# Optimization experiments

Hardware: AMD Instinct MI355X
Metric: run time of the kernel (lower is better)

Reference implementation:

```python
import jax, jax.numpy as jnp
import numpy as np

U = 128  # linear_units

def setup_inputs() -> dict:
    key = jax.random.key(0)
    k1, k2, k3, k4, k5, k6 = jax.random.split(key, 6)
    B, S, D = 16, 2048, 128
    x = jax.random.normal(k1, (B, S, D), dtype=jnp.float32)
    t = jax.random.uniform(k2, (B, S), dtype=jnp.float32)
    # glorot_uniform inits
    lim_qk = np.sqrt(6.0 / (D + U)).astype(np.float32)
    Wq = jax.random.uniform(k3, (D, U), minval=-lim_qk, maxval=lim_qk, dtype=jnp.float32)
    Wk = jax.random.uniform(k4, (D, U), minval=-lim_qk, maxval=lim_qk, dtype=jnp.float32)
    lim_s = np.sqrt(6.0 / (1 + S)).astype(np.float32)
    theta = jax.random.uniform(k5, (1, S), minval=-lim_s, maxval=lim_s, dtype=jnp.float32)
    mu = jax.random.uniform(k6, (1, S), minval=-lim_s, maxval=lim_s, dtype=jnp.float32)
    return {"x": x, "t": t, "Wq": Wq, "Wk": Wk, "theta": theta, "mu": mu}

def reference(x, t, Wq, Wk, theta, mu):
    # x: (B,S,D), t: (B,S), theta/mu: (1,S)
    scale = jnp.sqrt(jnp.asarray(U, dtype=x.dtype))
    q = x @ Wq                                   # (B,S,U)
    k = x @ Wk                                   # (B,S,U)
    scores = jnp.einsum('biu,bju->bij', q, k) / scale  # (B,S,S)
    alphas = jax.nn.softmax(scores, axis=-1)
    gn = jnp.einsum('bij,bjd->bid', alphas, x)   # weighted sum == alphas @ x, (B,S,D)
    time_fact = jax.nn.sigmoid(theta - mu * t)   # (B,S)
    v = jnp.sum(gn * time_fact[:, :, None], axis=1)  # (B,D)
    return v
```

## Files before the change

kernel.cpp:

```cpp
#include <hip/hip_runtime.h>
#include <hip/hip_bf16.h>

#define SS 2048
#define DD 128
#define BB 16
#define LDST 136
#define SCT 268

typedef short bf16x8 __attribute__((ext_vector_type(8)));
typedef float f32x4 __attribute__((ext_vector_type(4)));
typedef unsigned short ushort_t;

#define SB0() __builtin_amdgcn_sched_barrier(0)
#define WAITV(n) asm volatile("s_waitcnt vmcnt(" #n ")" ::: "memory")

__device__ __forceinline__ unsigned short f2bf(float f) {
  union { float f; unsigned u; } v; v.f = f;
  unsigned r = v.u + 0x7fffu + ((v.u >> 16) & 1u);
  return (unsigned short)(r >> 16);
}
__device__ __forceinline__ float fexp2(float x) { return __builtin_amdgcn_exp2f(x); }


__global__ __launch_bounds__(256) void wprep(
    const float* __restrict__ Wq, const float* __restrict__ Wk,
    ushort_t* __restrict__ wt_g) {
  int idx = blockIdx.x * 256 + threadIdx.x;
  int r = idx & 16383, uu = r >> 7, d = r & 127;
  if (idx < 16384)
    wt_g[uu * 128 + d] = f2bf(Wq[d * 128 + uu] * 0.1275174346f);
  else
    wt_g[(uu + 128) * 128 + d] = f2bf(Wk[d * 128 + uu]);
}

__global__ __launch_bounds__(256, 2) void qk_gemm(
    const float* __restrict__ x, const ushort_t* __restrict__ wt_g,
    uint4* __restrict__ qF, uint4* __restrict__ kF) {
  __shared__ ushort_t xs[64 * LDST];
  __shared__ ushort_t sc[64 * SCT];
  const int tid = threadIdx.x, wave = tid >> 6, lane = tid & 63;
  const int lq = lane & 15, quad = lane >> 4;
  const int m0 = blockIdx.x * 64;

#pragma unroll
  for (int i = 0; i < 8; ++i) {
    int idx = i * 256 + tid;
    int row = idx >> 5, c4 = (idx & 31) * 4;
    const float4 v = *(const float4*)(x + (size_t)(m0 + row) * DD + c4);
    ushort4 h;
    h.x = f2bf(v.x); h.y = f2bf(v.y); h.z = f2bf(v.z); h.w = f2bf(v.w);
    *(ushort4*)(&xs[row * LDST + c4]) = h;
  }
  bf16x8 wf[4][4];
#pragma unroll
  for (int nt = 0; nt < 4; ++nt)
#pragma unroll
    for (int ks = 0; ks < 4; ++ks)
      wf[nt][ks] = *(const bf16x8*)(wt_g + (wave * 64 + nt * 16 + lq) * 128 + ks * 32 + quad * 8);
  __syncthreads();

  f32x4 acc[4][4];
#pragma unroll
  for (int mt = 0; mt < 4; ++mt)
#pragma unroll
    for (int nt = 0; nt < 4; ++nt) acc[mt][nt] = (f32x4){0.f, 0.f, 0.f, 0.f};
#pragma unroll
  for (int mt = 0; mt < 4; ++mt) {
    bf16x8 af[4];
#pragma unroll
    for (int ks = 0; ks < 4; ++ks)
      af[ks] = *(const bf16x8*)(&xs[(mt * 16 + lq) * LDST + ks * 32 + quad * 8]);
#pragma unroll
    for (int nt = 0; nt < 4; ++nt)
#pragma unroll
      for (int ks = 0; ks < 4; ++ks)
        acc[mt][nt] = __builtin_amdgcn_mfma_f32_16x16x32_bf16(af[ks], wf[nt][ks], acc[mt][nt], 0, 0, 0);
  }
#pragma unroll
  for (int mt = 0; mt < 4; ++mt)
#pragma unroll
    for (int nt = 0; nt < 4; ++nt)
#pragma unroll
      for (int r = 0; r < 4; ++r)
        sc[(mt * 16 + quad * 4 + r) * SCT + wave * 64 + nt * 16 + lq] = f2bf(acc[mt][nt][r]);
  __syncthreads();
#pragma unroll
  for (int i = 0; i < 8; ++i) {
    int c = i * 256 + tid;
    int lane_c = c & 63, ks_c = (c >> 6) & 3, g_c = (c >> 8) & 3, isk = c >> 10;
    int li = lane_c & 15, qd = lane_c >> 4;
    int col = isk * 128 + ks_c * 32 + qd * 8;
    uint4 v = *(const uint4*)(&sc[(g_c * 16 + li) * SCT + col]);
    size_t G = (size_t)blockIdx.x * 4 + g_c;
    uint4* dst = isk ? kF : qF;
    dst[(G * 4 + ks_c) * 64 + lane_c] = v;
  }
}

__global__ __launch_bounds__(256, 2) void attn_fused(
    const uint4* __restrict__ qF, const uint4* __restrict__ kF,
    const float* __restrict__ t, const float* __restrict__ theta,
    const float* __restrict__ mu, float* __restrict__ w) {
  const int xcd = blockIdx.x & 7, s = blockIdx.x >> 3;
  const int b = xcd + ((s >> 5) << 3);
  const int ib = s & 31;
  const int i0 = ib * 64;
  const int tid = threadIdx.x, wave = tid >> 6, lane = tid & 63;
  const int lq = lane & 15, quad = lane >> 4;

  __shared__ float rs_lds[4][64];
  __shared__ float c_lds[64];

  const bf16x8* qc = (const bf16x8*)qF;

  bf16x8 af[4][4];
#pragma unroll
  for (int mt = 0; mt < 4; ++mt)
#pragma unroll
    for (int ks = 0; ks < 4; ++ks)
      af[mt][ks] = qc[((size_t)(b * 128 + ib * 4 + mt) * 4 + ks) * 64 + lane];

  const bf16x8* kb = (const bf16x8*)kF + (size_t)b * 128 * 4 * 64 + lane;
  auto loadg = [&](bf16x8 (&f)[4], int g) {
#pragma unroll
    for (int ks = 0; ks < 4; ++ks)
      f[ks] = kb[((size_t)g * 4 + ks) * 64];
  };
  auto G = [&](int m) { return (m >> 1) * 8 + wave * 2 + (m & 1); };

  const f32x4 z4 = {0.f, 0.f, 0.f, 0.f};
  auto mfma16 = [&](f32x4 (&a)[4], bf16x8 (&f)[4]) {
    __builtin_amdgcn_s_setprio(1);
#pragma unroll
    for (int mt = 0; mt < 4; ++mt)
      a[mt] = __builtin_amdgcn_mfma_f32_16x16x32_bf16(af[mt][0], f[0], z4, 0, 0, 0);
#pragma unroll
    for (int ks = 1; ks < 4; ++ks)
#pragma unroll
      for (int mt = 0; mt < 4; ++mt)
        a[mt] = __builtin_amdgcn_mfma_f32_16x16x32_bf16(af[mt][ks], f[ks], a[mt], 0, 0, 0);
    __builtin_amdgcn_s_setprio(0);
  };

  float rowsum[4][4];
#pragma unroll
  for (int mt = 0; mt < 4; ++mt)
#pragma unroll
    for (int r = 0; r < 4; ++r) rowsum[mt][r] = 0.f;
  auto proc1 = [&](f32x4 (&a)[4]) {
#pragma unroll
    for (int mt = 0; mt < 4; ++mt)
#pragma unroll
      for (int r = 0; r < 4; ++r) rowsum[mt][r] += fexp2(a[mt][r]);
  };

  bf16x8 fA[4], fB[4];
  f32x4 a[4];

  loadg(fA, G(0));
  loadg(fB, G(1));
  for (int m = 0; m < 30; m += 2) {
    WAITV(4); SB0();
    mfma16(a, fA);
    loadg(fA, G(m + 2)); SB0();
    proc1(a);
    WAITV(4); SB0();
    mfma16(a, fB);
    loadg(fB, G(m + 3)); SB0();
    proc1(a);
  }
  WAITV(4); SB0(); mfma16(a, fA); SB0(); proc1(a);
  WAITV(0); SB0(); mfma16(a, fB); SB0(); proc1(a);

#pragma unroll
  for (int d2 = 1; d2 <= 8; d2 <<= 1)
#pragma unroll
    for (int mt = 0; mt < 4; ++mt)
#pragma unroll
      for (int r = 0; r < 4; ++r)
        rowsum[mt][r] += __shfl_xor(rowsum[mt][r], d2, 64);
  if (lq == 0) {
#pragma unroll
    for (int mt = 0; mt < 4; ++mt)
#pragma unroll
      for (int r = 0; r < 4; ++r)
        rs_lds[wave][mt * 16 + quad * 4 + r] = rowsum[mt][r];
  }
  __syncthreads();
  if (tid < 64) {
    float l = rs_lds[0][tid] + rs_lds[1][tid] + rs_lds[2][tid] + rs_lds[3][tid];
    int gi = i0 + tid;
    float z = theta[gi] - mu[gi] * t[b * SS + gi];
    float tf = 1.f / (1.f + fexp2(-z * 1.44269504f));
    c_lds[tid] = tf / l;
  }
  __syncthreads();
  float creg[4][4];
#pragma unroll
  for (int mt = 0; mt < 4; ++mt)
#pragma unroll
    for (int r = 0; r < 4; ++r) creg[mt][r] = c_lds[mt * 16 + quad * 4 + r];

  auto proc2 = [&](f32x4 (&aa)[4], int g) {
    float cs = 0.f;
#pragma unroll
    for (int mt = 0; mt < 4; ++mt)
#pragma unroll
      for (int r = 0; r < 4; ++r) cs = fmaf(creg[mt][r], fexp2(aa[mt][r]), cs);
    cs += __shfl_xor(cs, 16, 64);
    cs += __shfl_xor(cs, 32, 64);
    if (lane < 16) atomicAdd(&w[b * SS + g * 16 + lane], cs);
  };

  loadg(fA, G(0));
  loadg(fB, G(1));
  for (int m = 0; m < 30; m += 2) {
    WAITV(4); SB0();
    mfma16(a, fA);
    loadg(fA, G(m + 2)); SB0();
    proc2(a, G(m));
    WAITV(4); SB0();
    mfma16(a, fB);
    loadg(fB, G(m + 3)); SB0();
    proc2(a, G(m + 1));
  }
  WAITV(4); SB0(); mfma16(a, fA); SB0(); proc2(a, G(30));
  WAITV(0); SB0(); mfma16(a, fB); SB0(); proc2(a, G(31));
}

__global__ __launch_bounds__(256) void finalize(
    const float* __restrict__ x, const float* __restrict__ w,
    float* __restrict__ out) {
  const int b = blockIdx.x >> 5;
  const int j0 = (blockIdx.x & 31) * 64;
  const int tid = threadIdx.x;
  const int d4 = (tid & 31) * 4, jo = tid >> 5;
  float4 a0 = {0.f, 0.f, 0.f, 0.f}, a1 = {0.f, 0.f, 0.f, 0.f};
#pragma unroll
  for (int jj = 0; jj < 4; ++jj) {
    int ja = j0 + jj * 16 + jo, jb = ja + 8;
    float wa = w[b * SS + ja], wb = w[b * SS + jb];
    const float4 xa = *(const float4*)(x + ((size_t)b * SS + ja) * DD + d4);
    const float4 xb = *(const float4*)(x + ((size_t)b * SS + jb) * DD + d4);
    a0.x = fmaf(wa, xa.x, a0.x); a0.y = fmaf(wa, xa.y, a0.y);
    a0.z = fmaf(wa, xa.z, a0.z); a0.w = fmaf(wa, xa.w, a0.w);
    a1.x = fmaf(wb, xb.x, a1.x); a1.y = fmaf(wb, xb.y, a1.y);
    a1.z = fmaf(wb, xb.z, a1.z); a1.w = fmaf(wb, xb.w, a1.w);
  }
  __shared__ float4 red[256];
  float4 acc = {a0.x + a1.x, a0.y + a1.y, a0.z + a1.z, a0.w + a1.w};
  red[tid] = acc;
  __syncthreads();
  if (tid < 128) {
    float4 o = red[tid + 128];
    red[tid].x += o.x; red[tid].y += o.y; red[tid].z += o.z; red[tid].w += o.w;
  }
  __syncthreads();
  if (tid < 64) {
    float4 o = red[tid + 64];
    red[tid].x += o.x; red[tid].y += o.y; red[tid].z += o.z; red[tid].w += o.w;
  }
  __syncthreads();
  if (tid < 32) {
    float4 v = red[tid], o = red[tid + 32];
    v.x += o.x; v.y += o.y; v.z += o.z; v.w += o.w;
    atomicAdd(&out[b * DD + d4 + 0], v.x);
    atomicAdd(&out[b * DD + d4 + 1], v.y);
    atomicAdd(&out[b * DD + d4 + 2], v.z);
    atomicAdd(&out[b * DD + d4 + 3], v.w);
  }
}

extern "C" void kernel_launch(void* const* d_in, const int* in_sizes, int n_in,
                              void* d_out, int out_size, void* d_ws, size_t ws_size,
                              hipStream_t stream) {
  const float* x = (const float*)d_in[0];
  const float* t = (const float*)d_in[1];
  const float* Wq = (const float*)d_in[2];
  const float* Wk = (const float*)d_in[3];
  const float* theta = (const float*)d_in[4];
  const float* mu = (const float*)d_in[5];
  float* out = (float*)d_out;

  uint4* qF = (uint4*)d_ws;
  uint4* kF = qF + (size_t)2048 * 4 * 64;
  ushort_t* wt_g = (ushort_t*)(kF + (size_t)2048 * 4 * 64);
  float* w = (float*)(wt_g + 256 * 128);

  hipMemsetAsync(w, 0, (size_t)BB * SS * sizeof(float), stream);
  hipMemsetAsync(d_out, 0, (size_t)BB * DD * sizeof(float), stream);

  wprep<<<dim3(128), dim3(256), 0, stream>>>(Wq, Wk, wt_g);
  qk_gemm<<<dim3(512), dim3(256), 0, stream>>>(x, wt_g, qF, kF);
  attn_fused<<<dim3(512), dim3(256), 0, stream>>>(qF, kF, t, theta, mu, w);
  finalize<<<dim3(512), dim3(256), 0, stream>>>(x, w, out);
}
```

Measured before the change: 127.2 us.

## Switch attention score MFMAs to 32x32x16 tiles with matching fragment layout

The attention kernel now uses 32x32x16 bf16 MFMA instructions instead of 16x16x32. The q/k fragment layout written by qk_gemm changes to match, and the row-sum and weight reductions are remapped to the 32-lane layout. Larger tiles reduce the instruction count and give more reuse per operand load, while the column atomics now cover 32 entries per wave step. Separately, wprep is rewritten as an LDS-tiled transpose over 8 blocks to coalesce weight reads. The costs are higher register pressure (8 K fragments per buffer, 16-float accumulators) and more complex index mapping.

```diff
diff --git a/kernel.cpp b/kernel.cpp
--- a/kernel.cpp
+++ b/kernel.cpp
@@ -9,6 +9,7 @@
 
 typedef short bf16x8 __attribute__((ext_vector_type(8)));
 typedef float f32x4 __attribute__((ext_vector_type(4)));
+typedef float f32x16 __attribute__((ext_vector_type(16)));
 typedef unsigned short ushort_t;
 
 #define SB0() __builtin_amdgcn_sched_barrier(0)
@@ -25,12 +26,29 @@
 __global__ __launch_bounds__(256) void wprep(
     const float* __restrict__ Wq, const float* __restrict__ Wk,
     ushort_t* __restrict__ wt_g) {
-  int idx = blockIdx.x * 256 + threadIdx.x;
-  int r = idx & 16383, uu = r >> 7, d = r & 127;
-  if (idx < 16384)
-    wt_g[uu * 128 + d] = f2bf(Wq[d * 128 + uu] * 0.1275174346f);
-  else
-    wt_g[(uu + 128) * 128 + d] = f2bf(Wk[d * 128 + uu]);
+  const int isK = blockIdx.x >> 2, ut = (blockIdx.x >> 1) & 1, dt = blockIdx.x & 1;
+  const int tid = threadIdx.x;
+  const float* W = isK ? Wk : Wq;
+  const float scale = isK ? 1.0f : 0.1275174346f;
+  __shared__ float tile[64][65];
+  {
+    int uu = tid & 63, dr = tid >> 6;
+#pragma unroll
+    for (int p = 0; p < 16; ++p) {
+      int d = p * 4 + dr;
+      tile[uu][d] = W[(size_t)(dt * 64 + d) * 128 + ut * 64 + uu];
+    }
+  }
+  __syncthreads();
+  {
+    int d = tid & 63, ur = tid >> 6;
+#pragma unroll
+    for (int p = 0; p < 16; ++p) {
+      int uu = p * 4 + ur;
+      wt_g[(size_t)(isK * 128 + ut * 64 + uu) * 128 + dt * 64 + d] =
+          f2bf(tile[uu][d] * scale);
+    }
+  }
 }
 
 __global__ __launch_bounds__(256, 2) void qk_gemm(
@@ -87,13 +105,13 @@
 #pragma unroll
   for (int i = 0; i < 8; ++i) {
     int c = i * 256 + tid;
-    int lane_c = c & 63, ks_c = (c >> 6) & 3, g_c = (c >> 8) & 3, isk = c >> 10;
-    int li = lane_c & 15, qd = lane_c >> 4;
-    int col = isk * 128 + ks_c * 32 + qd * 8;
-    uint4 v = *(const uint4*)(&sc[(g_c * 16 + li) * SCT + col]);
-    size_t G = (size_t)blockIdx.x * 4 + g_c;
+    int lane_c = c & 63, ci = c >> 6;
+    int wv = ci & 7, Hloc = (ci >> 3) & 1, isk = ci >> 4;
+    int row = Hloc * 32 + (lane_c & 31);
+    int col = isk * 128 + wv * 16 + (lane_c >> 5) * 8;
+    uint4 v = *(const uint4*)(&sc[row * SCT + col]);
     uint4* dst = isk ? kF : qF;
-    dst[(G * 4 + ks_c) * 64 + lane_c] = v;
+    dst[((size_t)(blockIdx.x * 2 + Hloc) * 8 + wv) * 64 + lane_c] = v;
   }
 }
 
@@ -106,85 +124,85 @@
   const int ib = s & 31;
   const int i0 = ib * 64;
   const int tid = threadIdx.x, wave = tid >> 6, lane = tid & 63;
-  const int lq = lane & 15, quad = lane >> 4;
+  const int l31 = lane & 31, lh = lane >> 5;
 
   __shared__ float rs_lds[4][64];
   __shared__ float c_lds[64];
 
   const bf16x8* qc = (const bf16x8*)qF;
-
-  bf16x8 af[4][4];
-#pragma unroll
-  for (int mt = 0; mt < 4; ++mt)
-#pragma unroll
-    for (int ks = 0; ks < 4; ++ks)
-      af[mt][ks] = qc[((size_t)(b * 128 + ib * 4 + mt) * 4 + ks) * 64 + lane];
-
-  const bf16x8* kb = (const bf16x8*)kF + (size_t)b * 128 * 4 * 64 + lane;
-  auto loadg = [&](bf16x8 (&f)[4], int g) {
-#pragma unroll
-    for (int ks = 0; ks < 4; ++ks)
-      f[ks] = kb[((size_t)g * 4 + ks) * 64];
+  bf16x8 af[2][8];
+#pragma unroll
+  for (int ht = 0; ht < 2; ++ht)
+#pragma unroll
+    for (int wv = 0; wv < 8; ++wv)
+      af[ht][wv] = qc[((size_t)(b * 64 + ib * 2 + ht) * 8 + wv) * 64 + lane];
+
+  const bf16x8* kb = (const bf16x8*)kF + (size_t)b * 64 * 8 * 64 + lane;
+  auto loadg = [&](bf16x8 (&f)[8], int hj) {
+#pragma unroll
+    for (int wv = 0; wv < 8; ++wv)
+      f[wv] = kb[((size_t)hj * 8 + wv) * 64];
   };
-  auto G = [&](int m) { return (m >> 1) * 8 + wave * 2 + (m & 1); };
-
-  const f32x4 z4 = {0.f, 0.f, 0.f, 0.f};
-  auto mfma16 = [&](f32x4 (&a)[4], bf16x8 (&f)[4]) {
+  auto HJ = [&](int m) { return m * 4 + wave; };
+
+  const f32x16 z16 = {0.f, 0.f, 0.f, 0.f, 0.f, 0.f, 0.f, 0.f,
+                      0.f, 0.f, 0.f, 0.f, 0.f, 0.f, 0.f, 0.f};
+  auto mfma32 = [&](f32x16 (&a)[2], bf16x8 (&f)[8]) {
     __builtin_amdgcn_s_setprio(1);
 #pragma unroll
-    for (int mt = 0; mt < 4; ++mt)
-      a[mt] = __builtin_amdgcn_mfma_f32_16x16x32_bf16(af[mt][0], f[0], z4, 0, 0, 0);
-#pragma unroll
-    for (int ks = 1; ks < 4; ++ks)
-#pragma unroll
-      for (int mt = 0; mt < 4; ++mt)
-        a[mt] = __builtin_amdgcn_mfma_f32_16x16x32_bf16(af[mt][ks], f[ks], a[mt], 0, 0, 0);
+    for (int ht = 0; ht < 2; ++ht)
+      a[ht] = __builtin_amdgcn_mfma_f32_32x32x16_bf16(af[ht][0], f[0], z16, 0, 0, 0);
+#pragma unroll
+    for (int wv = 1; wv < 8; ++wv)
+#pragma unroll
+      for (int ht = 0; ht < 2; ++ht)
+        a[ht] = __builtin_amdgcn_mfma_f32_32x32x16_bf16(af[ht][wv], f[wv], a[ht], 0, 0, 0);
     __builtin_amdgcn_s_setprio(0);
   };
 
-  float rowsum[4][4];
-#pragma unroll
-  for (int mt = 0; mt < 4; ++mt)
-#pragma unroll
-    for (int r = 0; r < 4; ++r) rowsum[mt][r] = 0.f;
-  auto proc1 = [&](f32x4 (&a)[4]) {
-#pragma unroll
-    for (int mt = 0; mt < 4; ++mt)
-#pragma unroll
-      for (int r = 0; r < 4; ++r) rowsum[mt][r] += fexp2(a[mt][r]);
+  float rowsum[2][16];
+#pragma unroll
+  for (int ht = 0; ht < 2; ++ht)
+#pragma unroll
+    for (int r = 0; r < 16; ++r) rowsum[ht][r] = 0.f;
+  auto proc1 = [&](f32x16 (&a)[2]) {
+#pragma unroll
+    for (int ht = 0; ht < 2; ++ht)
+#pragma unroll
+      for (int r = 0; r < 16; ++r) rowsum[ht][r] += fexp2(a[ht][r]);
   };
 
-  bf16x8 fA[4], fB[4];
-  f32x4 a[4];
-
-  loadg(fA, G(0));
-  loadg(fB, G(1));
-  for (int m = 0; m < 30; m += 2) {
-    WAITV(4); SB0();
-    mfma16(a, fA);
-    loadg(fA, G(m + 2)); SB0();
+  bf16x8 fA[8], fB[8];
+  f32x16 a[2];
+
+  loadg(fA, HJ(0));
+  loadg(fB, HJ(1));
+  for (int m = 0; m < 14; m += 2) {
+    WAITV(8); SB0();
+    mfma32(a, fA);
+    loadg(fA, HJ(m + 2)); SB0();
     proc1(a);
-    WAITV(4); SB0();
-    mfma16(a, fB);
-    loadg(fB, G(m + 3)); SB0();
+    WAITV(8); SB0();
+    mfma32(a, fB);
+    loadg(fB, HJ(m + 3)); SB0();
     proc1(a);
   }
-  WAITV(4); SB0(); mfma16(a, fA); SB0(); proc1(a);
-  WAITV(0); SB0(); mfma16(a, fB); SB0(); proc1(a);
-
-#pragma unroll
-  for (int d2 = 1; d2 <= 8; d2 <<= 1)
-#pragma unroll
-    for (int mt = 0; mt < 4; ++mt)
-#pragma unroll
-      for (int r = 0; r < 4; ++r)
-        rowsum[mt][r] += __shfl_xor(rowsum[mt][r], d2, 64);
-  if (lq == 0) {
-#pragma unroll
-    for (int mt = 0; mt < 4; ++mt)
-#pragma unroll
-      for (int r = 0; r < 4; ++r)
-        rs_lds[wave][mt * 16 + quad * 4 + r] = rowsum[mt][r];
+  WAITV(8); SB0(); mfma32(a, fA); SB0(); proc1(a);
+  WAITV(0); SB0(); mfma32(a, fB); SB0(); proc1(a);
+
+#pragma unroll
+  for (int d2 = 1; d2 <= 16; d2 <<= 1)
+#pragma unroll
+    for (int ht = 0; ht < 2; ++ht)
+#pragma unroll
+      for (int r = 0; r < 16; ++r)
+        rowsum[ht][r] += __shfl_xor(rowsum[ht][r], d2, 64);
+  if (l31 == 0) {
+#pragma unroll
+    for (int ht = 0; ht < 2; ++ht)
+#pragma unroll
+      for (int r = 0; r < 16; ++r)
+        rs_lds[wave][ht * 32 + (r & 3) + 8 * (r >> 2) + 4 * lh] = rowsum[ht][r];
   }
   __syncthreads();
   if (tid < 64) {
@@ -195,37 +213,39 @@
     c_lds[tid] = tf / l;
   }
   __syncthreads();
-  float creg[4][4];
-#pragma unroll
-  for (int mt = 0; mt < 4; ++mt)
-#pragma unroll
-    for (int r = 0; r < 4; ++r) creg[mt][r] = c_lds[mt * 16 + quad * 4 + r];
-
-  auto proc2 = [&](f32x4 (&aa)[4], int g) {
-    float cs = 0.f;
-#pragma unroll
-    for (int mt = 0; mt < 4; ++mt)
-#pragma unroll
-      for (int r = 0; r < 4; ++r) cs = fmaf(creg[mt][r], fexp2(aa[mt][r]), cs);
-    cs += __shfl_xor(cs, 16, 64);
+  float creg[2][16];
+#pragma unroll
+  for (int ht = 0; ht < 2; ++ht)
+#pragma unroll
+    for (int r = 0; r < 16; ++r)
+      creg[ht][r] = c_lds[ht * 32 + (r & 3) + 8 * (r >> 2) + 4 * lh];
+
+  auto proc2 = [&](f32x16 (&aa)[2], int hj) {
+    float c0 = 0.f, c1 = 0.f;
+#pragma unroll
+    for (int r = 0; r < 16; ++r) {
+      c0 = fmaf(creg[0][r], fexp2(aa[0][r]), c0);
+      c1 = fmaf(creg[1][r], fexp2(aa[1][r]), c1);
+    }
+    float cs = c0 + c1;
     cs += __shfl_xor(cs, 32, 64);
-    if (lane < 16) atomicAdd(&w[b * SS + g * 16 + lane], cs);
+    if (lane < 32) atomicAdd(&w[b * SS + hj * 32 + l31], cs);
   };
 
-  loadg(fA, G(0));
-  loadg(fB, G(1));
-  for (int m = 0; m < 30; m += 2) {
-    WAITV(4); SB0();
-    mfma16(a, fA);
-    loadg(fA, G(m + 2)); SB0();
-    proc2(a, G(m));
-    WAITV(4); SB0();
-    mfma16(a, fB);
-    loadg(fB, G(m + 3)); SB0();
-    proc2(a, G(m + 1));
-  }
-  WAITV(4); SB0(); mfma16(a, fA); SB0(); proc2(a, G(30));
-  WAITV(0); SB0(); mfma16(a, fB); SB0(); proc2(a, G(31));
+  loadg(fA, HJ(0));
+  loadg(fB, HJ(1));
+  for (int m = 0; m < 14; m += 2) {
+    WAITV(8); SB0();
+    mfma32(a, fA);
+    loadg(fA, HJ(m + 2)); SB0();
+    proc2(a, HJ(m));
+    WAITV(8); SB0();
+    mfma32(a, fB);
+    loadg(fB, HJ(m + 3)); SB0();
+    proc2(a, HJ(m + 1));
+  }
+  WAITV(8); SB0(); mfma32(a, fA); SB0(); proc2(a, HJ(14));
+  WAITV(0); SB0(); mfma32(a, fB); SB0(); proc2(a, HJ(15));
 }
 
 __global__ __launch_bounds__(256) void finalize(
@@ -283,14 +303,14 @@
   float* out = (float*)d_out;
 
   uint4* qF = (uint4*)d_ws;
-  uint4* kF = qF + (size_t)2048 * 4 * 64;
-  ushort_t* wt_g = (ushort_t*)(kF + (size_t)2048 * 4 * 64);
+  uint4* kF = qF + (size_t)16 * 64 * 8 * 64;
+  ushort_t* wt_g = (ushort_t*)(kF + (size_t)16 * 64 * 8 * 64);
   float* w = (float*)(wt_g + 256 * 128);
 
   hipMemsetAsync(w, 0, (size_t)BB * SS * sizeof(float), stream);
   hipMemsetAsync(d_out, 0, (size_t)BB * DD * sizeof(float), stream);
 
-  wprep<<<dim3(128), dim3(256), 0, stream>>>(Wq, Wk, wt_g);
+  wprep<<<dim3(8), dim3(256), 0, stream>>>(Wq, Wk, wt_g);
   qk_gemm<<<dim3(512), dim3(256), 0, stream>>>(x, wt_g, qF, kF);
   attn_fused<<<dim3(512), dim3(256), 0, stream>>>(qF, kF, t, theta, mu, w);
   finalize<<<dim3(512), dim3(256), 0, stream>>>(x, w, out);
```

New measurement: 129.7 us. Within noise of the previous version (+1.9%).
